# Performance work log

Measured on AMD Instinct MI355X. Metric: run time of the kernel, lower is better.

The kernel has to match this reference:

```python
import jax, jax.numpy as jnp
import numpy as np

NB_POOLS = 256


def setup_inputs() -> dict:
    key = jax.random.key(0)
    x = jax.random.normal(key, (32, 32, 32, 512), dtype=jnp.float32)
    return {"x": x}


def reference(x) -> jnp.ndarray:
    B, R, C, F = x.shape
    nb_maps = R * C
    x3 = x.reshape(B, nb_maps, F)
    # self-correlation: (B, nb_maps, nb_maps), normalized by feature count
    corr = jnp.einsum('bmf,bnf->bmn', x3, x3) / F
    corr = corr.reshape(B, R, C, nb_maps)
    # percentile ranks into the descending-sorted correlation values
    ranks = jnp.round(jnp.linspace(1.0, nb_maps - 1, NB_POOLS)).astype(jnp.int32)
    # full descending sort along last axis (matches tf.nn.top_k k=nb_maps)
    x_sort = -jnp.sort(-corr, axis=-1)
    x_pool = x_sort[..., ranks]  # (B, R, C, NB_POOLS)
    return x_pool
```

## Files before the change

kernel.cpp:

```cpp
#include <hip/hip_runtime.h>


#define NMAPS 1024
#define FDIM 512
#define TM 16
#define NT 256

typedef __attribute__((ext_vector_type(8))) short short8_t;
typedef __attribute__((ext_vector_type(4))) float f32x4;
typedef _Float16 h2 __attribute__((ext_vector_type(2)));

#define SELD 0x03020504u
#define SELA 0x07060100u

__device__ __forceinline__ h2 h2min(h2 a, h2 b) { return __builtin_elementwise_min(a, b); }
__device__ __forceinline__ h2 h2max(h2 a, h2 b) { return __builtin_elementwise_max(a, b); }

__device__ __forceinline__ unsigned h2u(h2 x) { union { h2 h; unsigned u; } t; t.h = x; return t.u; }
__device__ __forceinline__ h2 u2h(unsigned x) { union { h2 h; unsigned u; } t; t.u = x; return t.h; }

__device__ __forceinline__ h2 h2swap(h2 v) {
  unsigned u = h2u(v);
  return u2h((u >> 16) | (u << 16));
}

__device__ __forceinline__ h2 h2shfl_xor(h2 v, int m) {
  union { h2 h; int i; } u;
  u.h = v;
  u.i = __shfl_xor(u.i, m, 64);
  return u.h;
}

__device__ __forceinline__ void ce_pair(h2& a, h2& b, bool d) {
  h2 mn = h2min(a, b), mx = h2max(a, b);
  a = d ? mx : mn;
  b = d ? mn : mx;
}

__device__ __forceinline__ h2 ce1(h2 w, unsigned sel) {
  h2 s = h2swap(w);
  h2 mn = h2min(w, s), mx = h2max(w, s);
#if __has_builtin(__builtin_amdgcn_perm)
  return u2h(__builtin_amdgcn_perm(h2u(mx), h2u(mn), sel));
#else
  h2 rd; rd[0] = mx[0]; rd[1] = mn[1];
  h2 ra; ra[0] = mn[0]; ra[1] = mx[1];
  return (sel == SELD) ? rd : ra;
#endif
}

__device__ __forceinline__ void intra_merge16(h2 w[8], bool d, unsigned sel) {
  ce_pair(w[0], w[4], d); ce_pair(w[1], w[5], d); ce_pair(w[2], w[6], d); ce_pair(w[3], w[7], d);
  ce_pair(w[0], w[2], d); ce_pair(w[1], w[3], d); ce_pair(w[4], w[6], d); ce_pair(w[5], w[7], d);
  ce_pair(w[0], w[1], d); ce_pair(w[2], w[3], d); ce_pair(w[4], w[5], d); ce_pair(w[6], w[7], d);
#pragma unroll
  for (int u = 0; u < 8; ++u) w[u] = ce1(w[u], sel);
}

__device__ __forceinline__ void sort16(h2 w[8], bool d, unsigned sd, unsigned si) {
  w[0] = ce1(w[0], sd); w[1] = ce1(w[1], si); w[2] = ce1(w[2], sd); w[3] = ce1(w[3], si);
  w[4] = ce1(w[4], sd); w[5] = ce1(w[5], si); w[6] = ce1(w[6], sd); w[7] = ce1(w[7], si);
  ce_pair(w[0], w[1], d); ce_pair(w[2], w[3], !d); ce_pair(w[4], w[5], d); ce_pair(w[6], w[7], !d);
  w[0] = ce1(w[0], sd); w[1] = ce1(w[1], sd); w[2] = ce1(w[2], si); w[3] = ce1(w[3], si);
  w[4] = ce1(w[4], sd); w[5] = ce1(w[5], sd); w[6] = ce1(w[6], si); w[7] = ce1(w[7], si);
  ce_pair(w[0], w[2], d); ce_pair(w[1], w[3], d); ce_pair(w[4], w[6], !d); ce_pair(w[5], w[7], !d);
  ce_pair(w[0], w[1], d); ce_pair(w[2], w[3], d); ce_pair(w[4], w[5], !d); ce_pair(w[6], w[7], !d);
  w[0] = ce1(w[0], sd); w[1] = ce1(w[1], sd); w[2] = ce1(w[2], sd); w[3] = ce1(w[3], sd);
  w[4] = ce1(w[4], si); w[5] = ce1(w[5], si); w[6] = ce1(w[6], si); w[7] = ce1(w[7], si);
  intra_merge16(w, d, sd);
}

__device__ __forceinline__ void merge32(h2 w[16], bool d) {
  const unsigned sel = d ? SELD : SELA;
#pragma unroll
  for (int u = 0; u < 8; ++u) ce_pair(w[u], w[u + 8], d);
#pragma unroll
  for (int u = 0; u < 16; ++u)
    if ((u & 4) == 0) ce_pair(w[u], w[u | 4], d);
#pragma unroll
  for (int u = 0; u < 16; ++u)
    if ((u & 2) == 0) ce_pair(w[u], w[u | 2], d);
#pragma unroll
  for (int u = 0; u < 16; ++u)
    if ((u & 1) == 0) ce_pair(w[u], w[u | 1], d);
#pragma unroll
  for (int u = 0; u < 16; ++u) w[u] = ce1(w[u], sel);
}

template<int N>
__device__ __forceinline__ void cross_ceN(h2* w, int m, bool keepmax) {
#pragma unroll
  for (int u = 0; u < N; ++u) {
    h2 p = h2shfl_xor(w[u], m);
    h2 mn = h2min(w[u], p), mx = h2max(w[u], p);
    w[u] = keepmax ? mx : mn;
  }
}
__device__ __forceinline__ void cross_ce(h2 w[8], int m, bool keepmax) {
  cross_ceN<8>(w, m, keepmax);
}

template<int K>
__device__ __forceinline__ void bitonic_stage(h2 w8[8], int lane) {
  const bool laneDesc = (K >= 16) ? ((lane & (K >> 4)) == 0) : true;
#pragma unroll
  for (int j = 512; j >= 16; j >>= 1) {
    if (j > (K >> 1)) continue;
    const int m = j >> 4;
    const bool keepmax = (((lane & m) == 0) == laneDesc);
#pragma unroll
    for (int u = 0; u < 8; ++u) {
      h2 p = h2shfl_xor(w8[u], m);
      h2 mn = h2min(w8[u], p), mx = h2max(w8[u], p);
      w8[u] = keepmax ? mx : mn;
    }
  }
#pragma unroll
  for (int j = 8; j >= 2; j >>= 1) {
    if (j > (K >> 1)) continue;
    const int jw = j >> 1;
#pragma unroll
    for (int u = 0; u < 8; ++u) {
      if ((u & jw) == 0) {
        const int v = u | jw;
        const bool desc = (K <= 8) ? (((2 * u) & K) == 0) : laneDesc;
        h2 mn = h2min(w8[u], w8[v]), mx = h2max(w8[u], w8[v]);
        w8[u] = desc ? mx : mn;
        w8[v] = desc ? mn : mx;
      }
    }
  }
#pragma unroll
  for (int u = 0; u < 8; ++u) {
    const bool desc = (K <= 8) ? (((2 * u) & K) == 0) : laneDesc;
    h2 s = h2swap(w8[u]);
    h2 mn = h2min(w8[u], s), mx = h2max(w8[u], s);
    h2 rd = (h2){mx[0], mn[1]};
    h2 ra = (h2){mn[0], mx[1]};
    w8[u] = desc ? rd : ra;
  }
}

template<int K>
__device__ __forceinline__ void bitonic_stage_tail2(h2 A[8], h2 B[8], int lane) {
  const bool laneDesc = ((lane & (K >> 4)) == 0);
#pragma unroll
  for (int j = 512; j >= 16; j >>= 1) {
    if (j > (K >> 1)) continue;
    const int m = j >> 4;
    const bool km = (((lane & m) == 0) == laneDesc);
    cross_ce(A, m, km);
    cross_ce(B, m, km);
  }
  const unsigned sel = laneDesc ? SELD : SELA;
  intra_merge16(A, laneDesc, sel);
  intra_merge16(B, laneDesc, sel);
}

__device__ __forceinline__ void run_bitonic(h2 w8[8], int lane) {
  bitonic_stage<2>(w8, lane);
  bitonic_stage<4>(w8, lane);
  bitonic_stage<8>(w8, lane);
  bitonic_stage<16>(w8, lane);
  bitonic_stage<32>(w8, lane);
  bitonic_stage<64>(w8, lane);
  bitonic_stage<128>(w8, lane);
  bitonic_stage<256>(w8, lane);
  bitonic_stage<512>(w8, lane);
  bitonic_stage<1024>(w8, lane);
}

__global__ __launch_bounds__(256) void cvt_bf16_kernel(const float* __restrict__ x,
                                                       short* __restrict__ xw, int n8) {
  int i = blockIdx.x * 256 + threadIdx.x;
  if (i >= n8) return;
  const float4* x4 = reinterpret_cast<const float4*>(x);
  float4 a = x4[i * 2], c = x4[i * 2 + 1];
  float f[8] = {a.x, a.y, a.z, a.w, c.x, c.y, c.z, c.w};
  union { short8_t v; short s[8]; } o;
#pragma unroll
  for (int j = 0; j < 8; ++j) {
    unsigned u = __float_as_uint(f[j]);
    u += 0x7fffu + ((u >> 16) & 1u);
    o.s[j] = (short)(u >> 16);
  }
  reinterpret_cast<short8_t*>(xw)[i] = o.v;
}

__global__ __launch_bounds__(512) void corr_gemm_tiled(const short* __restrict__ xw,
                                                       unsigned* __restrict__ corrW) {
  __shared__ short Asm[2][128 * 32];
  __shared__ short Bsm[2][128 * 32];
  const int tid = threadIdx.x;
  int b, tile;
  if (gridDim.x == 2048) {
    const int bid = blockIdx.x;
    const int xcd = bid & 7;
    const int j = bid >> 3;
    b = (j >> 6) * 8 + xcd;
    tile = j & 63;
  } else {
    b = blockIdx.x >> 6;
    tile = blockIdx.x & 63;
  }
  const int it = tile >> 3, jt = tile & 7;
  const int i0 = it * 128, j0 = jt * 128;
  const int lane = tid & 63;
  const int w = tid >> 6;
  const int lr = lane & 15;
  const int kg = lane >> 4;
  const short* Xb = xw + (size_t)b * NMAPS * FDIM;

  const int sr = tid >> 2;
  const int ss = (tid & 3) ^ ((sr >> 1) & 3);
  const int srcOff = sr * FDIM + ss * 8;
  const int dstOff = tid * 8;

  const int rowa = w * 16 + lr;
  const int aOff = rowa * 32 + (kg ^ ((rowa >> 1) & 3)) * 8;
  int bOff[8];
#pragma unroll
  for (int fn = 0; fn < 8; ++fn) {
    const int rowb = fn * 16 + lr;
    bOff[fn] = rowb * 32 + (kg ^ ((rowb >> 1) & 3)) * 8;
  }

  f32x4 acc[8];
#pragma unroll
  for (int fn = 0; fn < 8; ++fn) acc[fn] = (f32x4){0.f, 0.f, 0.f, 0.f};

#define STAGE(buf, kt)                                                                \
  {                                                                                   \
    const short* gA = Xb + (size_t)i0 * FDIM + srcOff + (kt) * 32;                    \
    const short* gB = Xb + (size_t)j0 * FDIM + srcOff + (kt) * 32;                    \
    __builtin_amdgcn_global_load_lds(                                                 \
        (const __attribute__((address_space(1))) unsigned*)gA,                        \
        (__attribute__((address_space(3))) unsigned*)(Asm[buf] + dstOff), 16, 0, 0);  \
    __builtin_amdgcn_global_load_lds(                                                 \
        (const __attribute__((address_space(1))) unsigned*)gB,                        \
        (__attribute__((address_space(3))) unsigned*)(Bsm[buf] + dstOff), 16, 0, 0);  \
  }
#define SBAR() __builtin_amdgcn_sched_barrier(0)
#define BARRIER()                      \
  {                                    \
    SBAR();                            \
    __builtin_amdgcn_s_barrier();      \
    SBAR();                            \
  }

  STAGE(0, 0);

  for (int kt = 0; kt < 16; ++kt) {
    const int cur = kt & 1;
    BARRIER();
    if (kt < 15) {
      STAGE(cur ^ 1, kt + 1);
      SBAR();
      asm volatile("s_waitcnt vmcnt(2)" ::: "memory");
    } else {
      SBAR();
      asm volatile("s_waitcnt vmcnt(0)" ::: "memory");
    }
    BARRIER();

    short8_t a = *reinterpret_cast<const short8_t*>(Asm[cur] + aOff);
    short8_t bf[8];
#pragma unroll
    for (int fn = 0; fn < 8; ++fn)
      bf[fn] = *reinterpret_cast<const short8_t*>(Bsm[cur] + bOff[fn]);
#pragma unroll
    for (int fn = 0; fn < 8; ++fn)
      acc[fn] = __builtin_amdgcn_mfma_f32_16x16x32_bf16(bf[fn], a, acc[fn], 0, 0, 0);
  }
#undef STAGE
#undef BARRIER
#undef SBAR

  {
    const bool D128 = ((jt & 1) == 0);
    const bool d64 = ((kg & 2) == 0);
    const bool d32 = ((kg & 1) == 0);
    h2 W[16];
#pragma unroll
    for (int fn = 0; fn < 8; ++fn) {
      W[2 * fn] = (h2){(_Float16)acc[fn][0], (_Float16)acc[fn][1]};
      W[2 * fn + 1] = (h2){(_Float16)acc[fn][2], (_Float16)acc[fn][3]};
    }
    sort16(W, true, SELD, SELA);
    sort16(W + 8, false, SELA, SELD);
    merge32(W, d32);
    cross_ceN<16>(W, 16, d32 == d64);
    merge32(W, d64);
    cross_ceN<16>(W, 32, d64 == D128);
    cross_ceN<16>(W, 16, d32 == D128);
    merge32(W, D128);
    const size_t roww = ((size_t)b * NMAPS + i0 + w * 16 + lr) * 512;
    const int wq = (j0 >> 1) + kg * 16;
    union { h2 h[4]; uint4 u; } s0, s1, s2, s3;
#pragma unroll
    for (int q = 0; q < 4; ++q) { s0.h[q] = W[q]; s1.h[q] = W[4 + q]; s2.h[q] = W[8 + q]; s3.h[q] = W[12 + q]; }
    *reinterpret_cast<uint4*>(corrW + roww + wq) = s0.u;
    *reinterpret_cast<uint4*>(corrW + roww + wq + 4) = s1.u;
    *reinterpret_cast<uint4*>(corrW + roww + wq + 8) = s2.u;
    *reinterpret_cast<uint4*>(corrW + roww + wq + 12) = s3.u;
  }
}

__global__ __launch_bounds__(256) void sort_rows_kernel(const unsigned* __restrict__ corrW,
                                                        float* __restrict__ out) {
  const int tid = threadIdx.x;
  const int lane = tid & 63;
  const int rA = blockIdx.x * 8 + (tid >> 6) * 2;
  const int rB = rA + 1;
  const uint4* pa = reinterpret_cast<const uint4*>(corrW + (size_t)rA * 512);
  const uint4* pb = reinterpret_cast<const uint4*>(corrW + (size_t)rB * 512);

  h2 A[8], B[8];
  {
    union { uint4 u; h2 h[4]; } t0, t1;
    t0.u = pa[lane * 2]; t1.u = pa[lane * 2 + 1];
    A[0] = t0.h[0]; A[1] = t0.h[1]; A[2] = t0.h[2]; A[3] = t0.h[3];
    A[4] = t1.h[0]; A[5] = t1.h[1]; A[6] = t1.h[2]; A[7] = t1.h[3];
    t0.u = pb[lane * 2]; t1.u = pb[lane * 2 + 1];
    B[0] = t0.h[0]; B[1] = t0.h[1]; B[2] = t0.h[2]; B[3] = t0.h[3];
    B[4] = t1.h[0]; B[5] = t1.h[1]; B[6] = t1.h[2]; B[7] = t1.h[3];
  }

  bitonic_stage_tail2<256>(A, B, lane);
  bitonic_stage_tail2<512>(A, B, lane);
  bitonic_stage_tail2<1024>(A, B, lane);

  float* oa = out + (size_t)rA * 256;
  float* ob = out + (size_t)rB * 256;
#pragma unroll
  for (int u = 0; u < 8; ++u) {
#pragma unroll
    for (int hh = 0; hh < 2; ++hh) {
      const int i = lane * 16 + 2 * u + hh;
      const int p = (int)rint((double)(i - 1) * (255.0 / 1022.0));
      const int rk = (int)rint(1.0 + (double)p * (1022.0 / 255.0));
      if (rk == i) {
        oa[p] = (float)A[u][hh] * (1.f / FDIM);
        ob[p] = (float)B[u][hh] * (1.f / FDIM);
      }
    }
  }
}

__global__ __launch_bounds__(NT) void selfcorr_mfma_kernel(const short* __restrict__ xw,
                                                           float* __restrict__ out) {
  __shared__ alignas(16) h2 SH[TM * 512];
  const int tid = threadIdx.x;
  const int b = blockIdx.y;
  const int m0 = blockIdx.x * TM;
  const int lane = tid & 63;
  const int wid = tid >> 6;
  const int lr = lane & 15;
  const int kg = lane >> 4;
  const int wc = wid * 256;
  const short* Xb = xw + (size_t)b * NMAPS * FDIM;

  f32x4 acc[16];
#pragma unroll
  for (int t = 0; t < 16; ++t) acc[t] = (f32x4){0.f, 0.f, 0.f, 0.f};

  for (int kk = 0; kk < 16; ++kk) {
    const short8_t* base = reinterpret_cast<const short8_t*>(Xb + kk * 32 + kg * 8);
    short8_t afrag = base[(size_t)(m0 + lr) * 64];
    short8_t bfrag[16];
#pragma unroll
    for (int t = 0; t < 16; ++t) bfrag[t] = base[(size_t)(wc + t * 16 + lr) * 64];
#pragma unroll
    for (int t = 0; t < 16; ++t)
      acc[t] = __builtin_amdgcn_mfma_f32_16x16x32_bf16(bfrag[t], afrag, acc[t], 0, 0, 0);
  }

  {
    const int xorv = (lr & 7) << 2;
#pragma unroll
    for (int t = 0; t < 16; ++t) {
      h2 lo = (h2){(_Float16)(acc[t][0] * (1.f / FDIM)), (_Float16)(acc[t][1] * (1.f / FDIM))};
      h2 hi = (h2){(_Float16)(acc[t][2] * (1.f / FDIM)), (_Float16)(acc[t][3] * (1.f / FDIM))};
      const int W = (wc >> 1) + t * 8 + kg * 2;
      const int phys = lr * 512 + (W ^ xorv);
      union { h2 h[2]; uint2 u; } pk;
      pk.h[0] = lo; pk.h[1] = hi;
      *reinterpret_cast<uint2*>(&SH[phys]) = pk.u;
    }
  }
  __syncthreads();

  const int rowbase = wid * 4;
  for (int rr = rowbase; rr < rowbase + 4; ++rr) {
    const int rx = (rr & 7) << 2;
    h2 w8[8];
#pragma unroll
    for (int q = 0; q < 2; ++q) {
      const int p4 = rr * 512 + ((lane * 8 + q * 4) ^ rx);
      union { uint4 u; h2 h[4]; } un;
      un.u = *reinterpret_cast<const uint4*>(&SH[p4]);
      w8[q * 4 + 0] = un.h[0]; w8[q * 4 + 1] = un.h[1];
      w8[q * 4 + 2] = un.h[2]; w8[q * 4 + 3] = un.h[3];
    }
    run_bitonic(w8, lane);
#pragma unroll
    for (int q = 0; q < 2; ++q) {
      const int p4 = rr * 512 + ((lane * 8 + q * 4) ^ rx);
      union { uint4 u; h2 h[4]; } un;
      un.h[0] = w8[q * 4 + 0]; un.h[1] = w8[q * 4 + 1];
      un.h[2] = w8[q * 4 + 2]; un.h[3] = w8[q * 4 + 3];
      *reinterpret_cast<uint4*>(&SH[p4]) = un.u;
    }
  }
  __builtin_amdgcn_wave_barrier();

#pragma unroll
  for (int i = 0; i < 16; ++i) {
    const int rr = rowbase + (i >> 2);
    const int p = lane + ((i & 3) << 6);
    const int rank = (int)rint(1.0 + (double)p * (1022.0 / 255.0));
    const int Wr = (rank >> 1) ^ ((rr & 7) << 2);
    h2 hv = SH[rr * 512 + Wr];
    out[((size_t)(b * NMAPS + m0 + rr) << 8) + p] = (float)hv[rank & 1];
  }
}

__device__ __forceinline__ int sw4(int row, int c4) {
  return (row << 8) | (c4 ^ ((c4 >> 3) & 7));
}
__device__ __forceinline__ void ce(float& a, float& b, bool desc) {
  float mn = fminf(a, b);
  float mx = fmaxf(a, b);
  a = desc ? mx : mn;
  b = desc ? mn : mx;
}

__global__ __launch_bounds__(NT) void selfcorr_pool_kernel(const float* __restrict__ x,
                                                           float* __restrict__ out) {
  __shared__ float lds[TM * NMAPS];
  float4* S4 = reinterpret_cast<float4*>(lds);
  const int tid = threadIdx.x;
  const int b = blockIdx.y;
  const int m0 = blockIdx.x * TM;
  const float4* Xb = reinterpret_cast<const float4*>(x) + (size_t)b * NMAPS * (FDIM / 4);

  float4* A4 = reinterpret_cast<float4*>(lds);
#pragma unroll
  for (int idx = tid; idx < TM * (FDIM / 4); idx += NT) {
    A4[idx] = Xb[(m0 + (idx >> 7)) * 128 + (idx & 127)];
  }
  __syncthreads();

  float acc[TM][4];
#pragma unroll
  for (int m = 0; m < TM; ++m)
#pragma unroll
    for (int j = 0; j < 4; ++j) acc[m][j] = 0.0f;

  float4 nb0 = Xb[(tid + 0) * 128];
  float4 nb1 = Xb[(tid + 256) * 128];
  float4 nb2 = Xb[(tid + 512) * 128];
  float4 nb3 = Xb[(tid + 768) * 128];
  for (int k4 = 0; k4 < 128; ++k4) {
    float4 b0 = nb0, b1 = nb1, b2 = nb2, b3 = nb3;
    const int kn = (k4 < 127) ? (k4 + 1) : 127;
    nb0 = Xb[(tid + 0) * 128 + kn];
    nb1 = Xb[(tid + 256) * 128 + kn];
    nb2 = Xb[(tid + 512) * 128 + kn];
    nb3 = Xb[(tid + 768) * 128 + kn];
#pragma unroll
    for (int m = 0; m < TM; ++m) {
      float4 a = A4[m * 128 + k4];
      acc[m][0] += a.x * b0.x + a.y * b0.y + a.z * b0.z + a.w * b0.w;
      acc[m][1] += a.x * b1.x + a.y * b1.y + a.z * b1.z + a.w * b1.w;
      acc[m][2] += a.x * b2.x + a.y * b2.y + a.z * b2.z + a.w * b2.w;
      acc[m][3] += a.x * b3.x + a.y * b3.y + a.z * b3.z + a.w * b3.w;
    }
  }
  __syncthreads();

#pragma unroll
  for (int m = 0; m < TM; ++m) {
#pragma unroll
    for (int j = 0; j < 4; ++j) {
      const int n = tid + (j << 8);
      lds[sw4(m, n >> 2) * 4 + (n & 3)] = acc[m][j] * (1.0f / FDIM);
    }
  }
  __syncthreads();

#pragma unroll
  for (int c = 0; c < 2; ++c) {
    const int cid = tid + (c << 8);
    const int row = cid >> 5;
    const int chunk = cid & 31;
    float r[32];
#pragma unroll
    for (int q = 0; q < 8; ++q) {
      float4 t = S4[sw4(row, (chunk << 3) + q)];
      r[q * 4 + 0] = t.x; r[q * 4 + 1] = t.y; r[q * 4 + 2] = t.z; r[q * 4 + 3] = t.w;
    }
    const bool D = ((chunk & 1) == 0);
#pragma unroll
    for (int k2 = 2; k2 <= 32; k2 <<= 1) {
#pragma unroll
      for (int j = k2 >> 1; j > 0; j >>= 1) {
#pragma unroll
        for (int i = 0; i < 32; ++i) {
          if ((i & j) == 0) ce(r[i], r[i | j], ((i & k2) == 0) ? D : !D);
        }
      }
    }
#pragma unroll
    for (int q = 0; q < 8; ++q) {
      S4[sw4(row, (chunk << 3) + q)] =
          make_float4(r[q * 4 + 0], r[q * 4 + 1], r[q * 4 + 2], r[q * 4 + 3]);
    }
  }
  __syncthreads();

  for (int k = 64; k <= NMAPS; k <<= 1) {
    for (int j = k >> 1; j >= 32; j >>= 1) {
      const int j4 = j >> 2;
      const int kq = k >> 2;
#pragma unroll
      for (int q = 0; q < 8; ++q) {
        const int g = tid + (q << 8);
        const int row = g >> 7;
        const int v = g & 127;
        const int i4 = ((v & ~(j4 - 1)) << 1) | (v & (j4 - 1));
        const bool desc = ((i4 & kq) == 0);
        const int ia = sw4(row, i4);
        const int ib = sw4(row, i4 + j4);
        float4 va = S4[ia];
        float4 vb = S4[ib];
        float4 lo, hi;
        lo.x = fminf(va.x, vb.x); hi.x = fmaxf(va.x, vb.x);
        lo.y = fminf(va.y, vb.y); hi.y = fmaxf(va.y, vb.y);
        lo.z = fminf(va.z, vb.z); hi.z = fmaxf(va.z, vb.z);
        lo.w = fminf(va.w, vb.w); hi.w = fmaxf(va.w, vb.w);
        S4[ia] = desc ? hi : lo;
        S4[ib] = desc ? lo : hi;
      }
      __syncthreads();
    }
#pragma unroll
    for (int c = 0; c < 2; ++c) {
      const int cid = tid + (c << 8);
      const int row = cid >> 5;
      const int chunk = cid & 31;
      const bool D = (((chunk << 5) & k) == 0);
      float r[32];
#pragma unroll
      for (int q = 0; q < 8; ++q) {
        float4 t = S4[sw4(row, (chunk << 3) + q)];
        r[q * 4 + 0] = t.x; r[q * 4 + 1] = t.y; r[q * 4 + 2] = t.z; r[q * 4 + 3] = t.w;
      }
#pragma unroll
      for (int j = 16; j > 0; j >>= 1) {
#pragma unroll
        for (int i = 0; i < 32; ++i) {
          if ((i & j) == 0) ce(r[i], r[i | j], D);
        }
      }
#pragma unroll
      for (int q = 0; q < 8; ++q) {
        S4[sw4(row, (chunk << 3) + q)] =
            make_float4(r[q * 4 + 0], r[q * 4 + 1], r[q * 4 + 2], r[q * 4 + 3]);
      }
    }
    __syncthreads();
  }

  const int p = tid;
  const int rank = (int)rint(1.0 + (double)p * (1022.0 / 255.0));
#pragma unroll
  for (int m = 0; m < TM; ++m) {
    out[((size_t)(b * NMAPS + m0 + m) << 8) + p] = lds[sw4(m, rank >> 2) * 4 + (rank & 3)];
  }
}

extern "C" void kernel_launch(void* const* d_in, const int* in_sizes, int n_in,
                              void* d_out, int out_size, void* d_ws, size_t ws_size,
                              hipStream_t stream) {
  const float* x = reinterpret_cast<const float*>(d_in[0]);
  float* out = reinterpret_cast<float*>(d_out);
  const int nelem = in_sizes[0];
  const int B = nelem / (NMAPS * FDIM);
  const size_t need_split = (size_t)nelem * 2 + (size_t)B * NMAPS * NMAPS * 2;
  if (ws_size >= need_split) {
    short* xw = reinterpret_cast<short*>(d_ws);
    unsigned* corrW = reinterpret_cast<unsigned*>((char*)d_ws + (size_t)nelem * 2);
    const int n8 = nelem / 8;
    hipLaunchKernelGGL(cvt_bf16_kernel, dim3((n8 + 255) / 256), dim3(256), 0, stream, x, xw, n8);
    hipLaunchKernelGGL(corr_gemm_tiled, dim3(64 * B), dim3(512), 0, stream, xw, corrW);
    hipLaunchKernelGGL(sort_rows_kernel, dim3(B * NMAPS / 8), dim3(256), 0, stream, corrW, out);
  } else if (ws_size >= (size_t)nelem * 2) {
    short* xw = reinterpret_cast<short*>(d_ws);
    const int n8 = nelem / 8;
    hipLaunchKernelGGL(cvt_bf16_kernel, dim3((n8 + 255) / 256), dim3(256), 0, stream, x, xw, n8);
    hipLaunchKernelGGL(selfcorr_mfma_kernel, dim3(NMAPS / TM, B), dim3(NT), 0, stream, xw, out);
  } else {
    hipLaunchKernelGGL(selfcorr_pool_kernel, dim3(NMAPS / TM, B), dim3(NT), 0, stream, x, out);
  }
}
```

Measured before the change: 154.5 us.

## Switch correlation GEMM to 32x32x16 MFMA with 256-thread blocks

The correlation GEMM now runs 4 waves per 128x128 tile instead of 8. Each wave computes a 32x128 strip using 32x32x16 bf16 MFMAs, and each thread issues two global-to-LDS loads per operand per stage. The in-register epilogue sort is rebuilt for the new accumulator layout: each lane sorts 64 fp16 values with a new merge64 and needs only one cross-lane exchange. This cuts LDS fragment reads and cross-lane shuffles per output, at the cost of more registers per thread and fewer waves to hide latency.

After: 153.1 us. Within noise of the previous version (-0.9%).

```diff
diff --git a/kernel.cpp b/kernel.cpp
--- a/kernel.cpp
+++ b/kernel.cpp
@@ -8,6 +8,7 @@
 
 typedef __attribute__((ext_vector_type(8))) short short8_t;
 typedef __attribute__((ext_vector_type(4))) float f32x4;
+typedef __attribute__((ext_vector_type(16))) float f32x16;
 typedef _Float16 h2 __attribute__((ext_vector_type(2)));
 
 #define SELD 0x03020504u
@@ -87,6 +88,26 @@
   for (int u = 0; u < 16; ++u) w[u] = ce1(w[u], sel);
 }
 
+__device__ __forceinline__ void merge64(h2 w[32], bool d) {
+  const unsigned sel = d ? SELD : SELA;
+#pragma unroll
+  for (int u = 0; u < 16; ++u) ce_pair(w[u], w[u + 16], d);
+#pragma unroll
+  for (int u = 0; u < 32; ++u)
+    if ((u & 8) == 0) ce_pair(w[u], w[u | 8], d);
+#pragma unroll
+  for (int u = 0; u < 32; ++u)
+    if ((u & 4) == 0) ce_pair(w[u], w[u | 4], d);
+#pragma unroll
+  for (int u = 0; u < 32; ++u)
+    if ((u & 2) == 0) ce_pair(w[u], w[u | 2], d);
+#pragma unroll
+  for (int u = 0; u < 32; ++u)
+    if ((u & 1) == 0) ce_pair(w[u], w[u | 1], d);
+#pragma unroll
+  for (int u = 0; u < 32; ++u) w[u] = ce1(w[u], sel);
+}
+
 template<int N>
 __device__ __forceinline__ void cross_ceN(h2* w, int m, bool keepmax) {
 #pragma unroll
@@ -187,7 +208,7 @@
   reinterpret_cast<short8_t*>(xw)[i] = o.v;
 }
 
-__global__ __launch_bounds__(512) void corr_gemm_tiled(const short* __restrict__ xw,
+__global__ __launch_bounds__(256) void corr_gemm_tiled(const short* __restrict__ xw,
                                                        unsigned* __restrict__ corrW) {
   __shared__ short Asm[2][128 * 32];
   __shared__ short Bsm[2][128 * 32];
@@ -207,38 +228,57 @@
   const int i0 = it * 128, j0 = jt * 128;
   const int lane = tid & 63;
   const int w = tid >> 6;
-  const int lr = lane & 15;
-  const int kg = lane >> 4;
+  const int lr32 = lane & 31;
+  const int hi = lane >> 5;
   const short* Xb = xw + (size_t)b * NMAPS * FDIM;
 
-  const int sr = tid >> 2;
-  const int ss = (tid & 3) ^ ((sr >> 1) & 3);
-  const int srcOff = sr * FDIM + ss * 8;
-  const int dstOff = tid * 8;
-
-  const int rowa = w * 16 + lr;
-  const int aOff = rowa * 32 + (kg ^ ((rowa >> 1) & 3)) * 8;
-  int bOff[8];
-#pragma unroll
-  for (int fn = 0; fn < 8; ++fn) {
-    const int rowb = fn * 16 + lr;
-    bOff[fn] = rowb * 32 + (kg ^ ((rowb >> 1) & 3)) * 8;
-  }
-
-  f32x4 acc[8];
-#pragma unroll
-  for (int fn = 0; fn < 8; ++fn) acc[fn] = (f32x4){0.f, 0.f, 0.f, 0.f};
-
-#define STAGE(buf, kt)                                                                \
-  {                                                                                   \
-    const short* gA = Xb + (size_t)i0 * FDIM + srcOff + (kt) * 32;                    \
-    const short* gB = Xb + (size_t)j0 * FDIM + srcOff + (kt) * 32;                    \
-    __builtin_amdgcn_global_load_lds(                                                 \
-        (const __attribute__((address_space(1))) unsigned*)gA,                        \
-        (__attribute__((address_space(3))) unsigned*)(Asm[buf] + dstOff), 16, 0, 0);  \
-    __builtin_amdgcn_global_load_lds(                                                 \
-        (const __attribute__((address_space(1))) unsigned*)gB,                        \
-        (__attribute__((address_space(3))) unsigned*)(Bsm[buf] + dstOff), 16, 0, 0);  \
+  int srcOff[2], dstOff[2];
+  {
+    const int idxs[2] = {tid, tid + 256};
+#pragma unroll
+    for (int rp = 0; rp < 2; ++rp) {
+      const int r = idxs[rp] >> 2;
+      const int s = (idxs[rp] & 3) ^ ((r >> 1) & 3);
+      srcOff[rp] = r * FDIM + s * 8;
+      dstOff[rp] = idxs[rp] * 8;
+    }
+  }
+
+  int aOff[2], bOff[4][2];
+  {
+    const int ra = w * 32 + lr32;
+#pragma unroll
+    for (int ks = 0; ks < 2; ++ks)
+      aOff[ks] = ra * 32 + (((2 * ks + hi) ^ ((ra >> 1) & 3)) * 8);
+#pragma unroll
+    for (int tc = 0; tc < 4; ++tc) {
+      const int rb = tc * 32 + lr32;
+#pragma unroll
+      for (int ks = 0; ks < 2; ++ks)
+        bOff[tc][ks] = rb * 32 + (((2 * ks + hi) ^ ((rb >> 1) & 3)) * 8);
+    }
+  }
+
+  f32x16 acc[4];
+#pragma unroll
+  for (int tc = 0; tc < 4; ++tc)
+#pragma unroll
+    for (int q = 0; q < 16; ++q) acc[tc][q] = 0.f;
+
+#define STAGE(buf, kt)                                                                 \
+  {                                                                                    \
+    _Pragma("unroll") for (int rp = 0; rp < 2; ++rp) {                                 \
+      const short* gA = Xb + (size_t)i0 * FDIM + srcOff[rp] + (kt) * 32;               \
+      const short* gB = Xb + (size_t)j0 * FDIM + srcOff[rp] + (kt) * 32;               \
+      __builtin_amdgcn_global_load_lds(                                                \
+          (const __attribute__((address_space(1))) unsigned*)gA,                       \
+          (__attribute__((address_space(3))) unsigned*)(Asm[buf] + dstOff[rp]), 16,    \
+          0, 0);                                                                       \
+      __builtin_amdgcn_global_load_lds(                                                \
+          (const __attribute__((address_space(1))) unsigned*)gB,                       \
+          (__attribute__((address_space(3))) unsigned*)(Bsm[buf] + dstOff[rp]), 16,    \
+          0, 0);                                                                       \
+    }                                                                                  \
   }
 #define SBAR() __builtin_amdgcn_sched_barrier(0)
 #define BARRIER()                      \
@@ -256,53 +296,55 @@
     if (kt < 15) {
       STAGE(cur ^ 1, kt + 1);
       SBAR();
-      asm volatile("s_waitcnt vmcnt(2)" ::: "memory");
+      asm volatile("s_waitcnt vmcnt(4)" ::: "memory");
     } else {
       SBAR();
       asm volatile("s_waitcnt vmcnt(0)" ::: "memory");
     }
     BARRIER();
 
-    short8_t a = *reinterpret_cast<const short8_t*>(Asm[cur] + aOff);
-    short8_t bf[8];
-#pragma unroll
-    for (int fn = 0; fn < 8; ++fn)
-      bf[fn] = *reinterpret_cast<const short8_t*>(Bsm[cur] + bOff[fn]);
-#pragma unroll
-    for (int fn = 0; fn < 8; ++fn)
-      acc[fn] = __builtin_amdgcn_mfma_f32_16x16x32_bf16(bf[fn], a, acc[fn], 0, 0, 0);
+#pragma unroll
+    for (int ks = 0; ks < 2; ++ks) {
+      short8_t a = *reinterpret_cast<const short8_t*>(Asm[cur] + aOff[ks]);
+      short8_t bf[4];
+#pragma unroll
+      for (int tc = 0; tc < 4; ++tc)
+        bf[tc] = *reinterpret_cast<const short8_t*>(Bsm[cur] + bOff[tc][ks]);
+#pragma unroll
+      for (int tc = 0; tc < 4; ++tc)
+        acc[tc] = __builtin_amdgcn_mfma_f32_32x32x16_bf16(bf[tc], a, acc[tc], 0, 0, 0);
+    }
   }
 #undef STAGE
 #undef BARRIER
 #undef SBAR
 
   {
-    const bool D128 = ((jt & 1) == 0);
-    const bool d64 = ((kg & 2) == 0);
-    const bool d32 = ((kg & 1) == 0);
-    h2 W[16];
-#pragma unroll
-    for (int fn = 0; fn < 8; ++fn) {
-      W[2 * fn] = (h2){(_Float16)acc[fn][0], (_Float16)acc[fn][1]};
-      W[2 * fn + 1] = (h2){(_Float16)acc[fn][2], (_Float16)acc[fn][3]};
-    }
+    const bool D = ((jt & 1) == 0);
+    h2 W[32];
+#pragma unroll
+    for (int tc = 0; tc < 4; ++tc)
+#pragma unroll
+      for (int q = 0; q < 8; ++q)
+        W[tc * 8 + q] = (h2){(_Float16)acc[tc][2 * q], (_Float16)acc[tc][2 * q + 1]};
     sort16(W, true, SELD, SELA);
     sort16(W + 8, false, SELA, SELD);
-    merge32(W, d32);
-    cross_ceN<16>(W, 16, d32 == d64);
-    merge32(W, d64);
-    cross_ceN<16>(W, 32, d64 == D128);
-    cross_ceN<16>(W, 16, d32 == D128);
-    merge32(W, D128);
-    const size_t roww = ((size_t)b * NMAPS + i0 + w * 16 + lr) * 512;
-    const int wq = (j0 >> 1) + kg * 16;
-    union { h2 h[4]; uint4 u; } s0, s1, s2, s3;
-#pragma unroll
-    for (int q = 0; q < 4; ++q) { s0.h[q] = W[q]; s1.h[q] = W[4 + q]; s2.h[q] = W[8 + q]; s3.h[q] = W[12 + q]; }
-    *reinterpret_cast<uint4*>(corrW + roww + wq) = s0.u;
-    *reinterpret_cast<uint4*>(corrW + roww + wq + 4) = s1.u;
-    *reinterpret_cast<uint4*>(corrW + roww + wq + 8) = s2.u;
-    *reinterpret_cast<uint4*>(corrW + roww + wq + 12) = s3.u;
+    merge32(W, true);
+    sort16(W + 16, true, SELD, SELA);
+    sort16(W + 24, false, SELA, SELD);
+    merge32(W + 16, false);
+    merge64(W, hi == 0);
+    cross_ceN<32>(W, 32, (hi == 0) == D);
+    merge64(W, D);
+    const size_t roww = ((size_t)b * NMAPS + i0 + w * 32 + lr32) * 512;
+    const int wq = (j0 >> 1) + hi * 32;
+#pragma unroll
+    for (int g = 0; g < 8; ++g) {
+      union { h2 h[4]; uint4 u; } s;
+#pragma unroll
+      for (int q = 0; q < 4; ++q) s.h[q] = W[g * 4 + q];
+      *reinterpret_cast<uint4*>(corrW + roww + wq + g * 4) = s.u;
+    }
   }
 }
 
@@ -593,7 +635,7 @@
     unsigned* corrW = reinterpret_cast<unsigned*>((char*)d_ws + (size_t)nelem * 2);
     const int n8 = nelem / 8;
     hipLaunchKernelGGL(cvt_bf16_kernel, dim3((n8 + 255) / 256), dim3(256), 0, stream, x, xw, n8);
-    hipLaunchKernelGGL(corr_gemm_tiled, dim3(64 * B), dim3(512), 0, stream, xw, corrW);
+    hipLaunchKernelGGL(corr_gemm_tiled, dim3(64 * B), dim3(256), 0, stream, xw, corrW);
     hipLaunchKernelGGL(sort_rows_kernel, dim3(B * NMAPS / 8), dim3(256), 0, stream, corrW, out);
   } else if (ws_size >= (size_t)nelem * 2) {
     short* xw = reinterpret_cast<short*>(d_ws);
```
